# Kernel optimization log

Measured on AMD Instinct MI355X. Metric: run time of the kernel, lower is better.

Reference implementation:

```python
import jax, jax.numpy as jnp
import numpy as np

N_NODES = 100000
N_EDGES = 800000
IN_DIM = 128
NUM_HEADS = 8
HEAD_DIM = 16  # out_dim // num_heads = 128 // 8


def setup_inputs() -> dict:
    key = jax.random.key(0)
    ks = jax.random.split(key, 10)
    scale = 1.0 / np.sqrt(IN_DIM)
    return {
        "x": jax.random.normal(ks[0], (N_NODES, IN_DIM), dtype=jnp.float32),
        "edge_index": jax.random.randint(ks[1], (2, N_EDGES), 0, N_NODES, dtype=jnp.int64),
        "virt_h": jax.random.normal(ks[2], (1, IN_DIM), dtype=jnp.float32),
        "virt_edge_index": jax.random.randint(ks[3], (2, 1), 0, 1, dtype=jnp.int64),
        "Wq": jax.random.normal(ks[4], (IN_DIM, NUM_HEADS * HEAD_DIM), dtype=jnp.float32) * scale,
        "bq": jnp.zeros((NUM_HEADS * HEAD_DIM,), dtype=jnp.float32),
        "Wk": jax.random.normal(ks[5], (IN_DIM, NUM_HEADS * HEAD_DIM), dtype=jnp.float32) * scale,
        "bk": jnp.zeros((NUM_HEADS * HEAD_DIM,), dtype=jnp.float32),
        "Wv": jax.random.normal(ks[6], (IN_DIM, NUM_HEADS * HEAD_DIM), dtype=jnp.float32) * scale,
        "bv": jnp.zeros((NUM_HEADS * HEAD_DIM,), dtype=jnp.float32),
    }


def reference(x, edge_index, virt_h, virt_edge_index, Wq, bq, Wk, bk, Wv, bv):
    # use_virt_nodes=False: virt_h / virt_edge_index are unused dummies.
    n = x.shape[0]
    H, D = NUM_HEADS, HEAD_DIM
    Q = (x @ Wq + bq).reshape(n, H, D)
    K = (x @ Wk + bk).reshape(n, H, D)
    V = (x @ Wv + bv).reshape(n, H, D)

    src = edge_index[0]
    dst = edge_index[1]

    # edge-wise gather QK dot -> clamp -> exp; score: [E, H, 1]
    dot = jnp.sum(K[src] * Q[dst], axis=-1, keepdims=True) / np.sqrt(D).astype(np.float32)
    score = jnp.exp(jnp.clip(dot, -5.0, 5.0))

    msg = V[src] * score  # [E, H, D]
    wV = jax.ops.segment_sum(msg, dst, num_segments=n)     # [N, H, D]
    Z = jax.ops.segment_sum(score, dst, num_segments=n)    # [N, H, 1]

    h_out = (wV / (Z + 1e-6)).reshape(n, H * D)
    return h_out
```

## Files before the change

kernel.cpp:

```cpp
#include <hip/hip_runtime.h>

#define IN_DIM   128
#define NH       8
#define HD       16
#define OUTD     128
#define QKVD     384
#define SH       7
#define NSORTB   64

typedef unsigned short ushort_t;
typedef unsigned int   uint_t;
typedef __bf16 bf16x8 __attribute__((ext_vector_type(8)));
typedef float  f32x4  __attribute__((ext_vector_type(4)));

__device__ __forceinline__ float bf2f(ushort_t u) {
    return __uint_as_float(((uint_t)u) << 16);
}
__device__ __forceinline__ ushort_t f2bf(float f) {
    uint_t u = __float_as_uint(f);
    u += 0x7FFFu + ((u >> 16) & 1u);
    return (ushort_t)(u >> 16);
}

__global__ __launch_bounds__(256) void prep_w(
    const float* __restrict__ Wq, const float* __restrict__ Wk,
    const float* __restrict__ Wv, ushort_t* __restrict__ Wt,
    unsigned long long* __restrict__ desc)
{
    __shared__ float ld[32][33];
    int mat  = blockIdx.x >> 4;
    int tile = blockIdx.x & 15;
    int k0 = (tile >> 2) * 32, c0 = (tile & 3) * 32;
    const float* W = (mat == 0) ? Wq : (mat == 1) ? Wk : Wv;
    int t = threadIdx.x;
    {
        int k = t >> 3, c4 = (t & 7) * 4;
        float4 f = *(const float4*)&W[(size_t)(k0 + k) * 128 + c0 + c4];
        ld[k][c4 + 0] = f.x; ld[k][c4 + 1] = f.y;
        ld[k][c4 + 2] = f.z; ld[k][c4 + 3] = f.w;
    }
    __syncthreads();
    {
        int c = t >> 3, kg = (t & 7) * 4;
        union { ushort_t h[4]; uint2 u; } o;
        o.h[0] = f2bf(ld[kg + 0][c]); o.h[1] = f2bf(ld[kg + 1][c]);
        o.h[2] = f2bf(ld[kg + 2][c]); o.h[3] = f2bf(ld[kg + 3][c]);
        *(uint2*)&Wt[((size_t)(mat * 128 + c0 + c)) * 128 + k0 + kg] = o.u;
    }
    int t0 = blockIdx.x * 256 + threadIdx.x;
    if (t0 < 128) desc[t0] = 0ULL;
}

__global__ __launch_bounds__(1024) void ebucketA(
    const int* __restrict__ ei, int* __restrict__ Hf, int* __restrict__ aux,
    uint_t* __restrict__ regions, int E, int NBC, int CH)
{
    __shared__ uint_t recs[12500];
    __shared__ int hist[1024];
    __shared__ int scn[1024];
    const int tid = threadIdx.x;
    const int blk = blockIdx.x;
    const int e0g = blk * CH;
    const int e1g = min(E, e0g + CH);
    const int m   = e1g - e0g;

    hist[tid] = 0;
    __syncthreads();
    for (int e = e0g + tid; e < e1g; e += 1024)
        atomicAdd(&hist[ei[E + e] >> SH], 1);
    __syncthreads();
    for (int b = tid; b < NBC; b += 1024)
        Hf[b * NSORTB + blk] = hist[b];
    scn[tid] = hist[tid];
    __syncthreads();
    for (int off = 1; off < 1024; off <<= 1) {
        int v = (tid >= off) ? scn[tid - off] : 0;
        __syncthreads();
        scn[tid] += v;
        __syncthreads();
    }
    int excl = scn[tid] - hist[tid];
    if (tid < NBC) aux[tid * NSORTB + blk] = excl;
    if (tid == 0)  aux[NBC * NSORTB + blk] = m;
    hist[tid] = excl;
    __syncthreads();
    for (int e = e0g + tid; e < e1g; e += 1024) {
        int d = ei[E + e];
        int src = ei[e];
        int slot = atomicAdd(&hist[d >> SH], 1);
        recs[slot] = (uint_t)src | ((uint_t)(d & 127) << 20);
    }
    __syncthreads();
    for (int s = tid; s < m; s += 1024)
        regions[(size_t)blk * CH + s] = recs[s];
}

__global__ __launch_bounds__(1024) void scan4(
    int* __restrict__ P, unsigned long long* __restrict__ desc, int NS)
{
    __shared__ int sdata[1024];
    __shared__ int s_prefix;
    int b  = blockIdx.x;
    int i0 = (b * 1024 + threadIdx.x) * 4;
    int4 v = {0, 0, 0, 0};
    if (i0 < NS) v = *(const int4*)&P[i0];
    int s = v.x + v.y + v.z + v.w;
    sdata[threadIdx.x] = s;
    __syncthreads();
    for (int off = 1; off < 1024; off <<= 1) {
        int t = (threadIdx.x >= off) ? sdata[threadIdx.x - off] : 0;
        __syncthreads();
        sdata[threadIdx.x] += t;
        __syncthreads();
    }
    int incl  = sdata[threadIdx.x];
    int total = sdata[1023];

    if (threadIdx.x == 0) {
        unsigned long long st1 = ((unsigned long long)((b == 0) ? 2 : 1) << 32)
                                 | (uint_t)total;
        __hip_atomic_store(&desc[b], st1, __ATOMIC_RELEASE, __HIP_MEMORY_SCOPE_AGENT);
        int prefix = 0;
        if (b > 0) {
            int bb = b - 1;
            for (;;) {
                unsigned long long d = __hip_atomic_load(
                    &desc[bb], __ATOMIC_ACQUIRE, __HIP_MEMORY_SCOPE_AGENT);
                uint_t st = (uint_t)(d >> 32);
                if (st == 0) continue;
                prefix += (int)(uint_t)(d & 0xFFFFFFFFu);
                if (st == 2) break;
                bb--;
            }
            __hip_atomic_store(&desc[b],
                ((unsigned long long)2 << 32) | (uint_t)(prefix + total),
                __ATOMIC_RELEASE, __HIP_MEMORY_SCOPE_AGENT);
        }
        s_prefix = prefix;
    }
    __syncthreads();
    if (i0 < NS) {
        int base = s_prefix + incl - s;
        int4 o;
        o.x = base;
        o.y = base + v.x;
        o.z = base + v.x + v.y;
        o.w = base + v.x + v.y + v.z;
        *(int4*)&P[i0] = o;
    }
}

__global__ __launch_bounds__(256) void efine(
    const uint_t* __restrict__ regions, const int* __restrict__ aux,
    const int* __restrict__ S,
    int* __restrict__ P, int* __restrict__ sorted_src,
    int N, int NBC, int CH)
{
    __shared__ int rl[64], ro[64], doff[64];
    __shared__ int cnt[128], scn2[128];
    __shared__ uint_t stage[4096];
    __shared__ int    sst[4096];
    const int tid = threadIdx.x;
    const int b   = blockIdx.x;
    const int base = S[b * NSORTB];

    if (tid < 64) {
        int r0 = aux[b * NSORTB + tid];
        int r1 = aux[(b + 1) * NSORTB + tid];
        ro[tid] = r0;
        rl[tid] = r1 - r0;
        doff[tid] = r1 - r0;
    }
    __syncthreads();
    for (int off = 1; off < 64; off <<= 1) {
        int v = (tid >= off && tid < 64) ? doff[tid - off] : 0;
        __syncthreads();
        if (tid < 64) doff[tid] += v;
        __syncthreads();
    }
    const int m = doff[63];

    {
        int r = tid >> 2, k = tid & 3;
        int dst0 = doff[r] - rl[r];
        int src0 = ro[r];
        int len  = rl[r];
        for (int i = k; i < len; i += 4)
            stage[dst0 + i] = regions[(size_t)r * CH + src0 + i];
    }
    __syncthreads();

    if (tid < 128) cnt[tid] = 0;
    __syncthreads();
    for (int i = tid; i < m; i += 256)
        atomicAdd(&cnt[stage[i] >> 20], 1);
    __syncthreads();
    if (tid < 128) scn2[tid] = cnt[tid];
    __syncthreads();
    for (int off = 1; off < 128; off <<= 1) {
        int v = (tid >= off && tid < 128) ? scn2[tid - off] : 0;
        __syncthreads();
        if (tid < 128) scn2[tid] += v;
        __syncthreads();
    }
    if (tid < 128) {
        int excl = scn2[tid] - cnt[tid];
        int n = b * 128 + tid;
        if (n < N) P[n] = base + excl;
        cnt[tid] = excl;
    }
    __syncthreads();
    for (int i = tid; i < m; i += 256) {
        uint_t r = stage[i];
        int pos = atomicAdd(&cnt[r >> 20], 1);
        sst[pos] = (int)(r & 0xFFFFFu);
    }
    __syncthreads();
    for (int i = tid; i < m; i += 256)
        sorted_src[base + i] = sst[i];
}

__global__ __launch_bounds__(384, 3) void gemm(
    const float* __restrict__ x, const ushort_t* __restrict__ Wt,
    const float* __restrict__ bq, const float* __restrict__ bk,
    const float* __restrict__ bv,
    ushort_t* __restrict__ qkv,
    int N, int ntiles)
{
    __shared__ ushort_t sh[8320];

    const int tid  = threadIdx.x;
    const int w    = tid >> 6;
    const int quad = (tid >> 4) & 3;
    const int l15  = tid & 15;
    const int colg = w << 6;

    bf16x8 bfr[4][4];
#pragma unroll
    for (int kt = 0; kt < 4; kt++)
#pragma unroll
        for (int cs = 0; cs < 4; cs++) {
            int col = colg + cs * 16 + l15;
            bfr[kt][cs] = *(const bf16x8*)&Wt[(size_t)col * 128 + kt * 32 + quad * 8];
        }

    const int mat = w >> 1;
    const float* Bp = (mat == 0) ? bq : (mat == 1) ? bk : bv;
    float bias[4];
#pragma unroll
    for (int cs = 0; cs < 4; cs++)
        bias[cs] = Bp[((w & 1) << 6) + cs * 16 + l15];

    for (int tile = blockIdx.x; tile < ntiles; tile += gridDim.x) {
        const int row0 = tile * 64;
        __syncthreads();

        for (int ch = tid; ch < 1024; ch += 384) {
            int row = ch >> 4;
            int kc  = ch & 15;
            int grow = row0 + row; if (grow > N - 1) grow = N - 1;
            const float* xp = x + (size_t)grow * IN_DIM + kc * 8;
            float4 f0 = *(const float4*)xp;
            float4 f1 = *(const float4*)(xp + 4);
            union { ushort_t h[8]; uint4 u; } tt;
            tt.h[0] = f2bf(f0.x); tt.h[1] = f2bf(f0.y);
            tt.h[2] = f2bf(f0.z); tt.h[3] = f2bf(f0.w);
            tt.h[4] = f2bf(f1.x); tt.h[5] = f2bf(f1.y);
            tt.h[6] = f2bf(f1.z); tt.h[7] = f2bf(f1.w);
            *(uint4*)&sh[(kc * 65 + row) * 8] = tt.u;
        }
        __syncthreads();

        f32x4 acc[4][4];
#pragma unroll
        for (int r = 0; r < 4; r++)
#pragma unroll
            for (int cs = 0; cs < 4; cs++) acc[r][cs] = (f32x4){0.f, 0.f, 0.f, 0.f};

#pragma unroll
        for (int kt = 0; kt < 4; kt++) {
            int kc = kt * 4 + quad;
            bf16x8 af[4];
#pragma unroll
            for (int r = 0; r < 4; r++)
                af[r] = *(const bf16x8*)&sh[(kc * 65 + r * 16 + l15) * 8];
#pragma unroll
            for (int r = 0; r < 4; r++)
#pragma unroll
                for (int cs = 0; cs < 4; cs++)
                    acc[r][cs] = __builtin_amdgcn_mfma_f32_16x16x32_bf16(
                        af[r], bfr[kt][cs], acc[r][cs], 0, 0, 0);
        }

#define EPS 392
#pragma unroll
        for (int qq = 0; qq < 4; qq++) {
            __syncthreads();
            int lrow = quad << 2;
#pragma unroll
            for (int cs = 0; cs < 4; cs++) {
                int col = (w << 6) + cs * 16 + l15;
#pragma unroll
                for (int reg = 0; reg < 4; reg++)
                    sh[(lrow + reg) * EPS + col] = f2bf(acc[qq][cs][reg] + bias[cs]);
            }
            __syncthreads();
#pragma unroll
            for (int i = 0; i < 2; i++) {
                int c = tid + i * 384;
                int row = c / 48;
                int col = (c % 48) * 8;
                int grow = row0 + qq * 16 + row;
                if (grow < N) {
                    uint4 val = *(const uint4*)&sh[row * EPS + col];
                    *(uint4*)&qkv[(size_t)grow * QKVD + col] = val;
                }
            }
        }
#undef EPS
    }
}

__global__ __launch_bounds__(256) void segment_attn(
    const ushort_t* __restrict__ qkv,
    const int* __restrict__ P, const int* __restrict__ sorted_src,
    float* __restrict__ out, int N, int E)
{
    int n = (blockIdx.x * 256 + threadIdx.x) >> 4;
    int g = threadIdx.x & 15;
    if (n >= N) return;
    int start = P[n];
    int end   = (n + 1 < N) ? P[n + 1] : E;
    int deg   = end - start;

    const uint_t* qrow = (const uint_t*)(qkv + (size_t)n * QKVD);
    uint4 qu = *(const uint4*)(qrow + g * 4);
    float q0 = bf2f((ushort_t)(qu.x & 0xFFFF)), q1 = bf2f((ushort_t)(qu.x >> 16));
    float q2 = bf2f((ushort_t)(qu.y & 0xFFFF)), q3 = bf2f((ushort_t)(qu.y >> 16));
    float q4 = bf2f((ushort_t)(qu.z & 0xFFFF)), q5 = bf2f((ushort_t)(qu.z >> 16));
    float q6 = bf2f((ushort_t)(qu.w & 0xFFFF)), q7 = bf2f((ushort_t)(qu.w >> 16));

    float a0 = 0.f, a1 = 0.f, a2 = 0.f, a3 = 0.f;
    float a4 = 0.f, a5 = 0.f, a6 = 0.f, a7 = 0.f, z = 0.f;

    int myidx = (g < deg) ? sorted_src[start + g] : 0;
    int wbase = (threadIdx.x & 63) & 48;

#define PROC(ku, vu)                                                       \
    {                                                                      \
        float p = bf2f((ushort_t)((ku).x & 0xFFFF)) * q0                   \
                + bf2f((ushort_t)((ku).x >> 16))    * q1                   \
                + bf2f((ushort_t)((ku).y & 0xFFFF)) * q2                   \
                + bf2f((ushort_t)((ku).y >> 16))    * q3                   \
                + bf2f((ushort_t)((ku).z & 0xFFFF)) * q4                   \
                + bf2f((ushort_t)((ku).z >> 16))    * q5                   \
                + bf2f((ushort_t)((ku).w & 0xFFFF)) * q6                   \
                + bf2f((ushort_t)((ku).w >> 16))    * q7;                  \
        p += __shfl_xor(p, 1);                                             \
        p = fminf(fmaxf(p * 0.25f, -5.f), 5.f);                            \
        float s = __expf(p);                                               \
        a0 += bf2f((ushort_t)((vu).x & 0xFFFF)) * s;                       \
        a1 += bf2f((ushort_t)((vu).x >> 16))    * s;                       \
        a2 += bf2f((ushort_t)((vu).y & 0xFFFF)) * s;                       \
        a3 += bf2f((ushort_t)((vu).y >> 16))    * s;                       \
        a4 += bf2f((ushort_t)((vu).z & 0xFFFF)) * s;                       \
        a5 += bf2f((ushort_t)((vu).z >> 16))    * s;                       \
        a6 += bf2f((ushort_t)((vu).w & 0xFFFF)) * s;                       \
        a7 += bf2f((ushort_t)((vu).w >> 16))    * s;                       \
        z += s;                                                            \
    }

    int cnt = (deg < 16) ? deg : 16;
    int t = 0;
    for (; t + 4 <= cnt; t += 4) {
        int s0 = __shfl(myidx, wbase + t);
        int s1 = __shfl(myidx, wbase + t + 1);
        int s2 = __shfl(myidx, wbase + t + 2);
        int s3 = __shfl(myidx, wbase + t + 3);
        const uint_t* kv0 = (const uint_t*)(qkv + (size_t)s0 * QKVD + 128);
        const uint_t* kv1 = (const uint_t*)(qkv + (size_t)s1 * QKVD + 128);
        const uint_t* kv2 = (const uint_t*)(qkv + (size_t)s2 * QKVD + 128);
        const uint_t* kv3 = (const uint_t*)(qkv + (size_t)s3 * QKVD + 128);
        uint4 ku0 = *(const uint4*)(kv0 + g * 4);
        uint4 ku1 = *(const uint4*)(kv1 + g * 4);
        uint4 ku2 = *(const uint4*)(kv2 + g * 4);
        uint4 ku3 = *(const uint4*)(kv3 + g * 4);
        uint4 vu0 = *(const uint4*)(kv0 + 64 + g * 4);
        uint4 vu1 = *(const uint4*)(kv1 + 64 + g * 4);
        uint4 vu2 = *(const uint4*)(kv2 + 64 + g * 4);
        uint4 vu3 = *(const uint4*)(kv3 + 64 + g * 4);
        PROC(ku0, vu0); PROC(ku1, vu1); PROC(ku2, vu2); PROC(ku3, vu3);
    }
    for (; t + 2 <= cnt; t += 2) {
        int s0 = __shfl(myidx, wbase + t);
        int s1 = __shfl(myidx, wbase + t + 1);
        const uint_t* kv0 = (const uint_t*)(qkv + (size_t)s0 * QKVD + 128);
        const uint_t* kv1 = (const uint_t*)(qkv + (size_t)s1 * QKVD + 128);
        uint4 ku0 = *(const uint4*)(kv0 + g * 4);
        uint4 ku1 = *(const uint4*)(kv1 + g * 4);
        uint4 vu0 = *(const uint4*)(kv0 + 64 + g * 4);
        uint4 vu1 = *(const uint4*)(kv1 + 64 + g * 4);
        PROC(ku0, vu0); PROC(ku1, vu1);
    }
    if (t < cnt) {
        int s0 = __shfl(myidx, wbase + t);
        const uint_t* kv0 = (const uint_t*)(qkv + (size_t)s0 * QKVD + 128);
        uint4 ku0 = *(const uint4*)(kv0 + g * 4);
        uint4 vu0 = *(const uint4*)(kv0 + 64 + g * 4);
        PROC(ku0, vu0);
    }
    for (int j = start + 16; j + 2 <= end; j += 2) {
        int s0 = sorted_src[j];
        int s1 = sorted_src[j + 1];
        const uint_t* kv0 = (const uint_t*)(qkv + (size_t)s0 * QKVD + 128);
        const uint_t* kv1 = (const uint_t*)(qkv + (size_t)s1 * QKVD + 128);
        uint4 ku0 = *(const uint4*)(kv0 + g * 4);
        uint4 ku1 = *(const uint4*)(kv1 + g * 4);
        uint4 vu0 = *(const uint4*)(kv0 + 64 + g * 4);
        uint4 vu1 = *(const uint4*)(kv1 + 64 + g * 4);
        PROC(ku0, vu0); PROC(ku1, vu1);
    }
    if (deg > 16 && ((deg - 16) & 1)) {
        int s0 = sorted_src[end - 1];
        const uint_t* kv0 = (const uint_t*)(qkv + (size_t)s0 * QKVD + 128);
        uint4 ku0 = *(const uint4*)(kv0 + g * 4);
        uint4 vu0 = *(const uint4*)(kv0 + 64 + g * 4);
        PROC(ku0, vu0);
    }
#undef PROC

    float inv = 1.f / (z + 1e-6f);
    f32x4 o0 = {a0 * inv, a1 * inv, a2 * inv, a3 * inv};
    f32x4 o1 = {a4 * inv, a5 * inv, a6 * inv, a7 * inv};
    float* ob = out + (size_t)n * OUTD + g * 8;
    __builtin_nontemporal_store(o0, (f32x4*)ob);
    __builtin_nontemporal_store(o1, (f32x4*)(ob + 4));
}

extern "C" void kernel_launch(void* const* d_in, const int* in_sizes, int n_in,
                              void* d_out, int out_size, void* d_ws, size_t ws_size,
                              hipStream_t stream) {
    const float* x  = (const float*)d_in[0];
    const int*   ei = (const int*)d_in[1];
    const float* Wq = (const float*)d_in[4];
    const float* bq = (const float*)d_in[5];
    const float* Wk = (const float*)d_in[6];
    const float* bk = (const float*)d_in[7];
    const float* Wv = (const float*)d_in[8];
    const float* bv = (const float*)d_in[9];
    float* out = (float*)d_out;

    const int N = in_sizes[0] / IN_DIM;
    const int E = in_sizes[1] / 2;
    const int NBC = (N + 127) >> 7;
    const int NS  = NBC * NSORTB;
    const int CH  = (E + NSORTB - 1) / NSORTB;

    char* wsb = (char*)d_ws;
    ushort_t* qkv = (ushort_t*)wsb;
    ushort_t* Wt  = qkv + (size_t)N * QKVD;
    int* Hf = (int*)(Wt + 384 * 128);
    unsigned long long* desc = (unsigned long long*)(Hf + NS);
    int* aux = (int*)((char*)desc + 1024);
    uint_t* regions = (uint_t*)(aux + (NBC + 1) * NSORTB);
    int* sorted = (int*)(regions + (size_t)NSORTB * CH);
    int* P = sorted + E;

    const int ntiles = (N + 63) / 64;
    const int NSB    = (NS + 4095) / 4096;

    prep_w<<<48, 256, 0, stream>>>(Wq, Wk, Wv, Wt, desc);
    ebucketA<<<NSORTB, 1024, 0, stream>>>(ei, Hf, aux, regions, E, NBC, CH);
    scan4<<<NSB, 1024, 0, stream>>>(Hf, desc, NS);
    efine<<<NBC, 256, 0, stream>>>(regions, aux, Hf, P, sorted, N, NBC, CH);
    gemm<<<512, 384, 0, stream>>>(x, Wt, bq, bk, bv, qkv, N, ntiles);
    segment_attn<<<((size_t)N * 16 + 255) / 256, 256, 0, stream>>>(
        qkv, P, sorted, out, N, E);
}
```

Before: 248.8 us.

## Fuse edge bucketing into GEMM launch and fold global scan into efine

After: 475.3 us. 91.1% more time.

```diff
diff --git a/kernel.cpp b/kernel.cpp
--- a/kernel.cpp
+++ b/kernel.cpp
@@ -48,77 +48,192 @@
         *(uint2*)&Wt[((size_t)(mat * 128 + c0 + c)) * 128 + k0 + kg] = o.u;
     }
     int t0 = blockIdx.x * 256 + threadIdx.x;
-    if (t0 < 128) desc[t0] = 0ULL;
-}
-
-__global__ __launch_bounds__(1024) void ebucketA(
-    const int* __restrict__ ei, int* __restrict__ Hf, int* __restrict__ aux,
-    uint_t* __restrict__ regions, int E, int NBC, int CH)
+    if (t0 < 1024) desc[t0] = 0ULL;
+}
+
+__global__ __launch_bounds__(384, 3) void fat_gemm_sort(
+    const float* __restrict__ x, const ushort_t* __restrict__ Wt,
+    const float* __restrict__ bq, const float* __restrict__ bk,
+    const float* __restrict__ bv, ushort_t* __restrict__ qkv,
+    const int* __restrict__ ei, int* __restrict__ aux,
+    uint_t* __restrict__ regions,
+    int N, int E, int ntiles, int NBC, int CH)
 {
-    __shared__ uint_t recs[12500];
-    __shared__ int hist[1024];
-    __shared__ int scn[1024];
+    __shared__ __align__(16) char smem[58448];
+
+    if (blockIdx.x < NSORTB) {
+        uint_t* recs = (uint_t*)smem;
+        int* hist    = (int*)(smem + 50000);
+        int* scn     = (int*)(smem + 54096);
+        const int tid = threadIdx.x;
+        const int blk = blockIdx.x;
+        const int e0g = blk * CH;
+        const int e1g = min(E, e0g + CH);
+        const int m   = e1g - e0g;
+
+        for (int i = tid; i < 1024; i += 384) hist[i] = 0;
+        __syncthreads();
+        for (int e = e0g + tid; e < e1g; e += 384)
+            atomicAdd(&hist[ei[E + e] >> SH], 1);
+        __syncthreads();
+        if (tid < 64) {
+            int base16 = tid * 16;
+            int loc[16]; int s = 0;
+#pragma unroll
+            for (int i = 0; i < 16; i++) { loc[i] = s; s += hist[base16 + i]; }
+            int incl = s;
+            for (int off = 1; off < 64; off <<= 1) {
+                int t = __shfl_up(incl, off);
+                if (tid >= off) incl += t;
+            }
+            int cexcl = incl - s;
+#pragma unroll
+            for (int i = 0; i < 16; i++) scn[base16 + i] = cexcl + loc[i];
+        }
+        __syncthreads();
+        for (int b = tid; b < NBC; b += 384) aux[b * NSORTB + blk] = scn[b];
+        if (tid == 0) aux[NBC * NSORTB + blk] = m;
+        __syncthreads();
+        for (int e = e0g + tid; e < e1g; e += 384) {
+            int d = ei[E + e];
+            int src = ei[e];
+            int slot = atomicAdd(&scn[d >> SH], 1);
+            recs[slot] = (uint_t)src | ((uint_t)(d & 127) << 20);
+        }
+        __syncthreads();
+        for (int s = tid; s < m; s += 384)
+            regions[(size_t)blk * CH + s] = recs[s];
+        return;
+    }
+
+    ushort_t* sh = (ushort_t*)smem;
+
+    const int tid  = threadIdx.x;
+    const int w    = tid >> 6;
+    const int quad = (tid >> 4) & 3;
+    const int l15  = tid & 15;
+    const int colg = w << 6;
+
+    bf16x8 bfr[4][4];
+#pragma unroll
+    for (int kt = 0; kt < 4; kt++)
+#pragma unroll
+        for (int cs = 0; cs < 4; cs++) {
+            int col = colg + cs * 16 + l15;
+            bfr[kt][cs] = *(const bf16x8*)&Wt[(size_t)col * 128 + kt * 32 + quad * 8];
+        }
+
+    const int mat = w >> 1;
+    const float* Bp = (mat == 0) ? bq : (mat == 1) ? bk : bv;
+    float bias[4];
+#pragma unroll
+    for (int cs = 0; cs < 4; cs++)
+        bias[cs] = Bp[((w & 1) << 6) + cs * 16 + l15];
+
+    const int gstride = (int)gridDim.x - NSORTB;
+    for (int tile = (int)blockIdx.x - NSORTB; tile < ntiles; tile += gstride) {
+        const int row0 = tile * 64;
+        __syncthreads();
+
+        for (int ch = tid; ch < 1024; ch += 384) {
+            int row = ch >> 4;
+            int kc  = ch & 15;
+            int grow = row0 + row; if (grow > N - 1) grow = N - 1;
+            const float* xp = x + (size_t)grow * IN_DIM + kc * 8;
+            float4 f0 = *(const float4*)xp;
+            float4 f1 = *(const float4*)(xp + 4);
+            union { ushort_t h[8]; uint4 u; } tt;
+            tt.h[0] = f2bf(f0.x); tt.h[1] = f2bf(f0.y);
+            tt.h[2] = f2bf(f0.z); tt.h[3] = f2bf(f0.w);
+            tt.h[4] = f2bf(f1.x); tt.h[5] = f2bf(f1.y);
+            tt.h[6] = f2bf(f1.z); tt.h[7] = f2bf(f1.w);
+            *(uint4*)&sh[(kc * 65 + row) * 8] = tt.u;
+        }
+        __syncthreads();
+
+        f32x4 acc[4][4];
+#pragma unroll
+        for (int r = 0; r < 4; r++)
+#pragma unroll
+            for (int cs = 0; cs < 4; cs++) acc[r][cs] = (f32x4){0.f, 0.f, 0.f, 0.f};
+
+#pragma unroll
+        for (int kt = 0; kt < 4; kt++) {
+            int kc = kt * 4 + quad;
+            bf16x8 af[4];
+#pragma unroll
+            for (int r = 0; r < 4; r++)
+                af[r] = *(const bf16x8*)&sh[(kc * 65 + r * 16 + l15) * 8];
+#pragma unroll
+            for (int r = 0; r < 4; r++)
+#pragma unroll
+                for (int cs = 0; cs < 4; cs++)
+                    acc[r][cs] = __builtin_amdgcn_mfma_f32_16x16x32_bf16(
+                        af[r], bfr[kt][cs], acc[r][cs], 0, 0, 0);
+        }
+
+#define EPS 392
+#pragma unroll
+        for (int qq = 0; qq < 4; qq++) {
+            __syncthreads();
+            int lrow = quad << 2;
+#pragma unroll
+            for (int cs = 0; cs < 4; cs++) {
+                int col = (w << 6) + cs * 16 + l15;
+#pragma unroll
+                for (int reg = 0; reg < 4; reg++)
+                    sh[(lrow + reg) * EPS + col] = f2bf(acc[qq][cs][reg] + bias[cs]);
+            }
+            __syncthreads();
+#pragma unroll
+            for (int i = 0; i < 2; i++) {
+                int c = tid + i * 384;
+                int row = c / 48;
+                int col = (c % 48) * 8;
+                int grow = row0 + qq * 16 + row;
+                if (grow < N) {
+                    uint4 val = *(const uint4*)&sh[row * EPS + col];
+                    *(uint4*)&qkv[(size_t)grow * QKVD + col] = val;
+                }
+            }
+        }
+#undef EPS
+    }
+}
+
+__global__ __launch_bounds__(256) void efine(
+    const uint_t* __restrict__ regions, const int* __restrict__ aux,
+    unsigned long long* __restrict__ desc,
+    int* __restrict__ P, int* __restrict__ sorted_src,
+    int N, int NBC, int CH)
+{
+    __shared__ int rl[64], ro[64], doff[64];
+    __shared__ int cnt[128], scn2[128];
+    __shared__ uint_t stage[4096];
+    __shared__ int    sst[4096];
+    __shared__ int s_base;
     const int tid = threadIdx.x;
-    const int blk = blockIdx.x;
-    const int e0g = blk * CH;
-    const int e1g = min(E, e0g + CH);
-    const int m   = e1g - e0g;
-
-    hist[tid] = 0;
-    __syncthreads();
-    for (int e = e0g + tid; e < e1g; e += 1024)
-        atomicAdd(&hist[ei[E + e] >> SH], 1);
-    __syncthreads();
-    for (int b = tid; b < NBC; b += 1024)
-        Hf[b * NSORTB + blk] = hist[b];
-    scn[tid] = hist[tid];
-    __syncthreads();
-    for (int off = 1; off < 1024; off <<= 1) {
-        int v = (tid >= off) ? scn[tid - off] : 0;
-        __syncthreads();
-        scn[tid] += v;
-        __syncthreads();
-    }
-    int excl = scn[tid] - hist[tid];
-    if (tid < NBC) aux[tid * NSORTB + blk] = excl;
-    if (tid == 0)  aux[NBC * NSORTB + blk] = m;
-    hist[tid] = excl;
-    __syncthreads();
-    for (int e = e0g + tid; e < e1g; e += 1024) {
-        int d = ei[E + e];
-        int src = ei[e];
-        int slot = atomicAdd(&hist[d >> SH], 1);
-        recs[slot] = (uint_t)src | ((uint_t)(d & 127) << 20);
-    }
-    __syncthreads();
-    for (int s = tid; s < m; s += 1024)
-        regions[(size_t)blk * CH + s] = recs[s];
-}
-
-__global__ __launch_bounds__(1024) void scan4(
-    int* __restrict__ P, unsigned long long* __restrict__ desc, int NS)
-{
-    __shared__ int sdata[1024];
-    __shared__ int s_prefix;
-    int b  = blockIdx.x;
-    int i0 = (b * 1024 + threadIdx.x) * 4;
-    int4 v = {0, 0, 0, 0};
-    if (i0 < NS) v = *(const int4*)&P[i0];
-    int s = v.x + v.y + v.z + v.w;
-    sdata[threadIdx.x] = s;
-    __syncthreads();
-    for (int off = 1; off < 1024; off <<= 1) {
-        int t = (threadIdx.x >= off) ? sdata[threadIdx.x - off] : 0;
-        __syncthreads();
-        sdata[threadIdx.x] += t;
-        __syncthreads();
-    }
-    int incl  = sdata[threadIdx.x];
-    int total = sdata[1023];
-
-    if (threadIdx.x == 0) {
+    const int b   = blockIdx.x;
+
+    if (tid < 64) {
+        int r0 = aux[b * NSORTB + tid];
+        int r1 = aux[(b + 1) * NSORTB + tid];
+        ro[tid] = r0;
+        rl[tid] = r1 - r0;
+        doff[tid] = r1 - r0;
+    }
+    __syncthreads();
+    for (int off = 1; off < 64; off <<= 1) {
+        int v = (tid >= off && tid < 64) ? doff[tid - off] : 0;
+        __syncthreads();
+        if (tid < 64) doff[tid] += v;
+        __syncthreads();
+    }
+    const int m = doff[63];
+
+    if (tid == 0) {
         unsigned long long st1 = ((unsigned long long)((b == 0) ? 2 : 1) << 32)
-                                 | (uint_t)total;
+                                 | (uint_t)m;
         __hip_atomic_store(&desc[b], st1, __ATOMIC_RELEASE, __HIP_MEMORY_SCOPE_AGENT);
         int prefix = 0;
         if (b > 0) {
@@ -133,52 +248,11 @@
                 bb--;
             }
             __hip_atomic_store(&desc[b],
-                ((unsigned long long)2 << 32) | (uint_t)(prefix + total),
+                ((unsigned long long)2 << 32) | (uint_t)(prefix + m),
                 __ATOMIC_RELEASE, __HIP_MEMORY_SCOPE_AGENT);
         }
-        s_prefix = prefix;
-    }
-    __syncthreads();
-    if (i0 < NS) {
-        int base = s_prefix + incl - s;
-        int4 o;
-        o.x = base;
-        o.y = base + v.x;
-        o.z = base + v.x + v.y;
-        o.w = base + v.x + v.y + v.z;
-        *(int4*)&P[i0] = o;
-    }
-}
-
-__global__ __launch_bounds__(256) void efine(
-    const uint_t* __restrict__ regions, const int* __restrict__ aux,
-    const int* __restrict__ S,
-    int* __restrict__ P, int* __restrict__ sorted_src,
-    int N, int NBC, int CH)
-{
-    __shared__ int rl[64], ro[64], doff[64];
-    __shared__ int cnt[128], scn2[128];
-    __shared__ uint_t stage[4096];
-    __shared__ int    sst[4096];
-    const int tid = threadIdx.x;
-    const int b   = blockIdx.x;
-    const int base = S[b * NSORTB];
-
-    if (tid < 64) {
-        int r0 = aux[b * NSORTB + tid];
-        int r1 = aux[(b + 1) * NSORTB + tid];
-        ro[tid] = r0;
-        rl[tid] = r1 - r0;
-        doff[tid] = r1 - r0;
-    }
-    __syncthreads();
-    for (int off = 1; off < 64; off <<= 1) {
-        int v = (tid >= off && tid < 64) ? doff[tid - off] : 0;
-        __syncthreads();
-        if (tid < 64) doff[tid] += v;
-        __syncthreads();
-    }
-    const int m = doff[63];
+        s_base = prefix;
+    }
 
     {
         int r = tid >> 2, k = tid & 3;
@@ -206,7 +280,7 @@
     if (tid < 128) {
         int excl = scn2[tid] - cnt[tid];
         int n = b * 128 + tid;
-        if (n < N) P[n] = base + excl;
+        if (n < N) P[n] = s_base + excl;
         cnt[tid] = excl;
     }
     __syncthreads();
@@ -217,108 +291,7 @@
     }
     __syncthreads();
     for (int i = tid; i < m; i += 256)
-        sorted_src[base + i] = sst[i];
-}
-
-__global__ __launch_bounds__(384, 3) void gemm(
-    const float* __restrict__ x, const ushort_t* __restrict__ Wt,
-    const float* __restrict__ bq, const float* __restrict__ bk,
-    const float* __restrict__ bv,
-    ushort_t* __restrict__ qkv,
-    int N, int ntiles)
-{
-    __shared__ ushort_t sh[8320];
-
-    const int tid  = threadIdx.x;
-    const int w    = tid >> 6;
-    const int quad = (tid >> 4) & 3;
-    const int l15  = tid & 15;
-    const int colg = w << 6;
-
-    bf16x8 bfr[4][4];
-#pragma unroll
-    for (int kt = 0; kt < 4; kt++)
-#pragma unroll
-        for (int cs = 0; cs < 4; cs++) {
-            int col = colg + cs * 16 + l15;
-            bfr[kt][cs] = *(const bf16x8*)&Wt[(size_t)col * 128 + kt * 32 + quad * 8];
-        }
-
-    const int mat = w >> 1;
-    const float* Bp = (mat == 0) ? bq : (mat == 1) ? bk : bv;
-    float bias[4];
-#pragma unroll
-    for (int cs = 0; cs < 4; cs++)
-        bias[cs] = Bp[((w & 1) << 6) + cs * 16 + l15];
-
-    for (int tile = blockIdx.x; tile < ntiles; tile += gridDim.x) {
-        const int row0 = tile * 64;
-        __syncthreads();
-
-        for (int ch = tid; ch < 1024; ch += 384) {
-            int row = ch >> 4;
-            int kc  = ch & 15;
-            int grow = row0 + row; if (grow > N - 1) grow = N - 1;
-            const float* xp = x + (size_t)grow * IN_DIM + kc * 8;
-            float4 f0 = *(const float4*)xp;
-            float4 f1 = *(const float4*)(xp + 4);
-            union { ushort_t h[8]; uint4 u; } tt;
-            tt.h[0] = f2bf(f0.x); tt.h[1] = f2bf(f0.y);
-            tt.h[2] = f2bf(f0.z); tt.h[3] = f2bf(f0.w);
-            tt.h[4] = f2bf(f1.x); tt.h[5] = f2bf(f1.y);
-            tt.h[6] = f2bf(f1.z); tt.h[7] = f2bf(f1.w);
-            *(uint4*)&sh[(kc * 65 + row) * 8] = tt.u;
-        }
-        __syncthreads();
-
-        f32x4 acc[4][4];
-#pragma unroll
-        for (int r = 0; r < 4; r++)
-#pragma unroll
-            for (int cs = 0; cs < 4; cs++) acc[r][cs] = (f32x4){0.f, 0.f, 0.f, 0.f};
-
-#pragma unroll
-        for (int kt = 0; kt < 4; kt++) {
-            int kc = kt * 4 + quad;
-            bf16x8 af[4];
-#pragma unroll
-            for (int r = 0; r < 4; r++)
-                af[r] = *(const bf16x8*)&sh[(kc * 65 + r * 16 + l15) * 8];
-#pragma unroll
-            for (int r = 0; r < 4; r++)
-#pragma unroll
-                for (int cs = 0; cs < 4; cs++)
-                    acc[r][cs] = __builtin_amdgcn_mfma_f32_16x16x32_bf16(
-                        af[r], bfr[kt][cs], acc[r][cs], 0, 0, 0);
-        }
-
-#define EPS 392
-#pragma unroll
-        for (int qq = 0; qq < 4; qq++) {
-            __syncthreads();
-            int lrow = quad << 2;
-#pragma unroll
-            for (int cs = 0; cs < 4; cs++) {
-                int col = (w << 6) + cs * 16 + l15;
-#pragma unroll
-                for (int reg = 0; reg < 4; reg++)
-                    sh[(lrow + reg) * EPS + col] = f2bf(acc[qq][cs][reg] + bias[cs]);
-            }
-            __syncthreads();
-#pragma unroll
-            for (int i = 0; i < 2; i++) {
-                int c = tid + i * 384;
-                int row = c / 48;
-                int col = (c % 48) * 8;
-                int grow = row0 + qq * 16 + row;
-                if (grow < N) {
-                    uint4 val = *(const uint4*)&sh[row * EPS + col];
-                    *(uint4*)&qkv[(size_t)grow * QKVD + col] = val;
-                }
-            }
-        }
-#undef EPS
-    }
+        sorted_src[s_base + i] = sst[i];
 }
 
 __global__ __launch_bounds__(256) void segment_attn(
@@ -453,27 +426,23 @@
     const int N = in_sizes[0] / IN_DIM;
     const int E = in_sizes[1] / 2;
     const int NBC = (N + 127) >> 7;
-    const int NS  = NBC * NSORTB;
     const int CH  = (E + NSORTB - 1) / NSORTB;
 
     char* wsb = (char*)d_ws;
     ushort_t* qkv = (ushort_t*)wsb;
     ushort_t* Wt  = qkv + (size_t)N * QKVD;
-    int* Hf = (int*)(Wt + 384 * 128);
-    unsigned long long* desc = (unsigned long long*)(Hf + NS);
-    int* aux = (int*)((char*)desc + 1024);
+    unsigned long long* desc = (unsigned long long*)(Wt + 384 * 128);
+    int* aux = (int*)(desc + 1024);
     uint_t* regions = (uint_t*)(aux + (NBC + 1) * NSORTB);
     int* sorted = (int*)(regions + (size_t)NSORTB * CH);
     int* P = sorted + E;
 
     const int ntiles = (N + 63) / 64;
-    const int NSB    = (NS + 4095) / 4096;
 
     prep_w<<<48, 256, 0, stream>>>(Wq, Wk, Wv, Wt, desc);
-    ebucketA<<<NSORTB, 1024, 0, stream>>>(ei, Hf, aux, regions, E, NBC, CH);
-    scan4<<<NSB, 1024, 0, stream>>>(Hf, desc, NS);
-    efine<<<NBC, 256, 0, stream>>>(regions, aux, Hf, P, sorted, N, NBC, CH);
-    gemm<<<512, 384, 0, stream>>>(x, Wt, bq, bk, bv, qkv, N, ntiles);
+    fat_gemm_sort<<<512, 384, 0, stream>>>(
+        x, Wt, bq, bk, bv, qkv, ei, aux, regions, N, E, ntiles, NBC, CH);
+    efine<<<NBC, 256, 0, stream>>>(regions, aux, desc, P, sorted, N, NBC, CH);
     segment_attn<<<((size_t)N * 16 + 255) / 256, 256, 0, stream>>>(
         qkv, P, sorted, out, N, E);
 }
```
